# Kernel tuning notes

Measured on AMD Instinct MI355X. Metric: run time of the kernel, lower is better.

The kernel has to match this reference:

```python
import jax, jax.numpy as jnp
import numpy as np

H, DK = 12, 64  # num_heads, key_size == head_size
NEG_BIG = 1e12


def setup_inputs() -> dict:
    key = jax.random.key(0)
    ks = jax.random.split(key, 10)
    B, S, D = 4, 1024, 768
    w = lambda k, shape: jax.random.normal(k, shape, jnp.float32) * 0.02
    return {
        'q': jax.random.normal(ks[0], (B, S, D), jnp.float32),
        'k': jax.random.normal(ks[1], (B, S, D), jnp.float32),
        'v': jax.random.normal(ks[2], (B, S, D), jnp.float32),
        'Wq': w(ks[3], (D, H * DK)), 'bq': jnp.zeros((H * DK,), jnp.float32),
        'Wk': w(ks[4], (D, H * DK)), 'bk': jnp.zeros((H * DK,), jnp.float32),
        'Wv': w(ks[5], (D, H * DK)), 'bv': jnp.zeros((H * DK,), jnp.float32),
        'Wo': w(ks[6], (H * DK, H * DK)), 'bo': jnp.zeros((H * DK,), jnp.float32),
        'pos_embeddings': w(ks[7], (S, S, DK)),
        'q_mask': jnp.ones((B, S), jnp.bool_),
        'v_mask': jnp.ones((B, S), jnp.bool_),
    }


def reference(q, k, v, Wq, bq, Wk, bk, Wv, bv, Wo, bo, pos_embeddings, q_mask, v_mask):
    B, Sq, _ = q.shape
    qm = q_mask.astype(q.dtype)  # [B, Sq]
    vm = v_mask.astype(q.dtype)  # [B, Sk]

    qw = (q @ Wq + bq).reshape(B, Sq, H, DK)
    kw = (k @ Wk + bk).reshape(B, -1, H, DK)
    vw = (v @ Wv + bv).reshape(B, -1, H, DK)

    # logits + typical_relative pre-softmax bias
    a = jnp.einsum('bjhd,bkhd->bhjk', qw, kw)
    a = a + jnp.einsum('bjhd,jkd->bhjk', qw, pos_embeddings)
    a = a / jnp.asarray(DK, a.dtype) ** 0.5

    # sequence_masking on key axis (additive -1e12 on padded keys)
    a = a - (1.0 - vm[:, None, None, :]) * NEG_BIG
    a = jax.nn.softmax(a, axis=-1)

    # AV + typical_relative post-softmax bias
    o = jnp.einsum('bhjk,bkhd->bjhd', a, vw)
    o = o + jnp.einsum('bhjk,jkd->bjhd', a, pos_embeddings)

    o = o.reshape(B, Sq, H * DK) @ Wo + bo
    # sequence_masking on query axis (multiplicative)
    return o * qm[:, :, None]
```

## Files before the change

kernel.cpp:

```cpp
#include <hip/hip_runtime.h>


typedef __attribute__((ext_vector_type(8))) short bf16x8;
typedef __attribute__((ext_vector_type(4))) float f32x4;

constexpr int kS = 1024, kH = 12, kHD = 768, kBH = 48;
#define SCALE 0.125f
#define MFMA16 __builtin_amdgcn_mfma_f32_16x16x32_bf16

#define GLOAD16(gp, lp)                                                     \
  __builtin_amdgcn_global_load_lds(                                         \
      (const __attribute__((address_space(1))) void*)(gp),                  \
      (__attribute__((address_space(3))) void*)(lp), 16, 0, 0)

__device__ inline ushort f2b(float f) {
  uint u = __builtin_bit_cast(uint, f);
  u += 0x7FFFu + ((u >> 16) & 1u);
  return (ushort)(u >> 16);
}
__device__ inline float b2f(ushort h) {
  return __builtin_bit_cast(float, ((uint)h) << 16);
}

__global__ __launch_bounds__(256) void cvt_all_k(
    const float* __restrict__ s0, const float* __restrict__ s1,
    const float* __restrict__ s2, ushort* __restrict__ d0,
    ushort* __restrict__ d1, ushort* __restrict__ d2,
    const float* __restrict__ W0, const float* __restrict__ W1,
    const float* __restrict__ W2, const float* __restrict__ W3,
    ushort* __restrict__ T0, ushort* __restrict__ T1,
    ushort* __restrict__ T2, ushort* __restrict__ T3)
{
  __shared__ ushort t[64][65];
  const int tid = threadIdx.x;
  const int z = blockIdx.y;
  if (z < 3) {
    const float* in = z == 0 ? s0 : z == 1 ? s1 : s2;
    ushort* out = z == 0 ? d0 : z == 1 ? d1 : d2;
    int i = blockIdx.x * 256 + tid;
    if (i >= 393216) return;
    const float4* p = (const float4*)(in + (size_t)i * 8);
    float4 a = p[0], b = p[1];
    ushort4 o0 = { f2b(a.x), f2b(a.y), f2b(a.z), f2b(a.w) };
    ushort4 o1 = { f2b(b.x), f2b(b.y), f2b(b.z), f2b(b.w) };
    ushort* q = out + (size_t)i * 8;
    *(ushort4*)q = o0; *(ushort4*)(q + 4) = o1;
    return;
  }
  int idx = blockIdx.x;
  if (idx >= 576) return;
  int wsel = idx / 144, tno = idx % 144;
  const float* W = wsel == 0 ? W0 : wsel == 1 ? W1 : wsel == 2 ? W2 : W3;
  ushort* Wt = wsel == 0 ? T0 : wsel == 1 ? T1 : wsel == 2 ? T2 : T3;
  int r0 = (tno / 12) * 64, c0 = (tno % 12) * 64;
#pragma unroll
  for (int it = 0; it < 4; ++it) {
    int i2 = it * 256 + tid;
    int r = i2 >> 4, c4 = (i2 & 15) << 2;
    float4 v = *(const float4*)(W + (size_t)(r0 + r) * kHD + c0 + c4);
    t[c4 + 0][r] = f2b(v.x); t[c4 + 1][r] = f2b(v.y);
    t[c4 + 2][r] = f2b(v.z); t[c4 + 3][r] = f2b(v.w);
  }
  __syncthreads();
#pragma unroll
  for (int it = 0; it < 4; ++it) {
    int i2 = it * 256 + tid;
    int rr = i2 >> 4, c4 = (i2 & 15) << 2;
    ushort4 o = { t[rr][c4 + 0], t[rr][c4 + 1], t[rr][c4 + 2], t[rr][c4 + 3] };
    *(ushort4*)(Wt + (size_t)(c0 + rr) * kHD + r0 + c4) = o;
  }
}

template <int SM>
__device__ __forceinline__ void gemm_nt_body(
    const ushort* __restrict__ A, const ushort* __restrict__ Bt,
    const float* __restrict__ bias, void* __restrict__ out, int N, int K)
{
  __shared__ ushort As[64 * 40];
  __shared__ ushort Bs[64 * 40];
  int tid = threadIdx.x, w = tid >> 6, l = tid & 63, lg = l >> 4, lr = l & 15;
  int wr = w >> 1, wc = w & 1;
  int m0 = blockIdx.y * 64;
  int n0 = blockIdx.x * 64;
  int sr = tid >> 2, sc = (tid & 3) * 8;
  f32x4 acc[2][2] = {};
  for (int kb = 0; kb < K; kb += 32) {
    __syncthreads();
    *(int4*)&As[sr * 40 + sc] = *(const int4*)&A[(size_t)(m0 + sr) * K + kb + sc];
    *(int4*)&Bs[sr * 40 + sc] = *(const int4*)&Bt[(size_t)(n0 + sr) * K + kb + sc];
    __syncthreads();
    bf16x8 A0 = *(const bf16x8*)&As[(wr * 32 + lr) * 40 + 8 * lg];
    bf16x8 A1 = *(const bf16x8*)&As[(wr * 32 + 16 + lr) * 40 + 8 * lg];
    bf16x8 B0 = *(const bf16x8*)&Bs[(wc * 32 + lr) * 40 + 8 * lg];
    bf16x8 B1 = *(const bf16x8*)&Bs[(wc * 32 + 16 + lr) * 40 + 8 * lg];
    acc[0][0] = MFMA16(A0, B0, acc[0][0], 0, 0, 0);
    acc[0][1] = MFMA16(A0, B1, acc[0][1], 0, 0, 0);
    acc[1][0] = MFMA16(A1, B0, acc[1][0], 0, 0, 0);
    acc[1][1] = MFMA16(A1, B1, acc[1][1], 0, 0, 0);
  }
#pragma unroll
  for (int mf = 0; mf < 2; ++mf)
#pragma unroll
    for (int nf = 0; nf < 2; ++nf) {
      int col = n0 + wc * 32 + nf * 16 + lr;
      float bs = bias[col];
      int row0 = m0 + wr * 32 + mf * 16 + 4 * lg;
      if constexpr (SM == 0) {
        ushort* o = (ushort*)out;
#pragma unroll
        for (int r = 0; r < 4; ++r)
          o[(size_t)(row0 + r) * N + col] = f2b(acc[mf][nf][r] + bs);
      } else if constexpr (SM == 1) {
        ushort* o = (ushort*)out;
        int b = row0 >> 10, ks = row0 & 1023;
        int h = col >> 6, dd = col & 63;
        int ph = (ks & ~63) + ((((ks >> 3) & 7) ^ (dd & 7)) << 3) + (ks & 7);
        ushort4 pk = { f2b(acc[mf][nf][0] + bs), f2b(acc[mf][nf][1] + bs),
                       f2b(acc[mf][nf][2] + bs), f2b(acc[mf][nf][3] + bs) };
        *(ushort4*)(o + ((size_t)((b * kH + h) * 64 + dd)) * kS + ph) = pk;
      } else if constexpr (SM == 3) {
        ushort* o = (ushort*)out;
        int d = col & 63, hh = col >> 6;
#pragma unroll
        for (int r = 0; r < 4; ++r) {
          int row = row0 + r;
          int dp = ((((d >> 3) ^ (row & 7)) << 3)) | (d & 7);
          o[(size_t)row * N + hh * 64 + dp] = f2b(acc[mf][nf][r] + bs);
        }
      } else {
        float* o = (float*)out;
#pragma unroll
        for (int r = 0; r < 4; ++r)
          o[(size_t)(row0 + r) * N + col] = acc[mf][nf][r] + bs;
      }
    }
}

__global__ __launch_bounds__(256) void gemm_qkv_proj_k(
    const ushort* __restrict__ qb, const ushort* __restrict__ kb,
    const ushort* __restrict__ vb,
    const ushort* __restrict__ Wqt, const ushort* __restrict__ Wkt,
    const ushort* __restrict__ Wvt,
    const float* __restrict__ bq, const float* __restrict__ bk,
    const float* __restrict__ bv,
    ushort* __restrict__ qw, ushort* __restrict__ kw, ushort* __restrict__ vwT)
{
  if (blockIdx.z == 0)      gemm_nt_body<0>(qb, Wqt, bq, qw, kHD, kHD);
  else if (blockIdx.z == 1) gemm_nt_body<3>(kb, Wkt, bk, kw, kHD, kHD);
  else                      gemm_nt_body<1>(vb, Wvt, bv, vwT, kHD, kHD);
}
__global__ __launch_bounds__(256) void gemm_out_k(
    const ushort* __restrict__ ob, const ushort* __restrict__ Wot,
    const float* __restrict__ bo, float* __restrict__ out)
{
  gemm_nt_body<2>(ob, Wot, bo, out, kHD, kHD);
}

__global__ __launch_bounds__(512) void logits_pos_k(
    const ushort* __restrict__ qw, const float* __restrict__ pos,
    ushort* __restrict__ lbuf, ushort* __restrict__ posb)
{
  __shared__ ushort Qs[48 * 72];
  __shared__ ushort Ps[256 * 72];
  const int tid = threadIdx.x;
  const int w = tid >> 6, l = tid & 63, lg = l >> 4, lr = l & 15;
  const int j = blockIdx.x;
  const int jk = j & 7;

  for (int i = tid; i < 48 * 16; i += 512) {
    int bh = i >> 4, c4 = (i & 15) * 4;
    int b = bh / kH, h = bh - b * kH;
    ushort4 v = *(const ushort4*)&qw[((size_t)(b * kS + j)) * kHD + h * 64 + c4];
    *(ushort4*)&Qs[bh * 72 + c4] = v;
  }

  for (int kt = 0; kt < 4; ++kt) {
    const int k0 = kt * 256;
    __syncthreads();
    const float* psrc = pos + ((size_t)j * kS + k0) * 64;
    for (int i = tid; i < 256 * 16; i += 512) {
      int kk = i >> 4, c4 = (i & 15) * 4;
      float4 v = *(const float4*)(psrc + kk * 64 + c4);
      ushort4 o = { f2b(v.x), f2b(v.y), f2b(v.z), f2b(v.w) };
      *(ushort4*)&Ps[kk * 72 + c4] = o;
    }
    __syncthreads();

    f32x4 acc[3][2] = {};
#pragma unroll
    for (int s = 0; s < 2; ++s) {
      bf16x8 A[3], Bv[2];
#pragma unroll
      for (int mf = 0; mf < 3; ++mf)
        A[mf] = *(const bf16x8*)&Qs[(mf * 16 + lr) * 72 + s * 32 + 8 * lg];
#pragma unroll
      for (int nf = 0; nf < 2; ++nf)
        Bv[nf] = *(const bf16x8*)&Ps[(w * 32 + nf * 16 + lr) * 72 + s * 32 + 8 * lg];
#pragma unroll
      for (int mf = 0; mf < 3; ++mf)
#pragma unroll
        for (int nf = 0; nf < 2; ++nf)
          acc[mf][nf] = MFMA16(A[mf], Bv[nf], acc[mf][nf], 0, 0, 0);
    }
    for (int i = tid; i < 2048; i += 512) {
      int row = i >> 3, seg = i & 7;
      *(int4*)&posb[((size_t)j * kS + k0 + row) * 64 + seg * 8] =
          *(const int4*)&Ps[row * 72 + seg * 8];
    }
    __syncthreads();
    ushort* Ct = Ps;
#pragma unroll
    for (int mf = 0; mf < 3; ++mf)
#pragma unroll
      for (int nf = 0; nf < 2; ++nf)
#pragma unroll
        for (int r = 0; r < 4; ++r)
          Ct[(mf * 16 + 4 * lg + r) * 264 + w * 32 + nf * 16 + lr] =
              f2b(acc[mf][nf][r] * SCALE);
    __syncthreads();
    for (int i = tid; i < 48 * 32; i += 512) {
      int row = i >> 5, seg = i & 31;
      int ph = (seg >> 3) * 64 + (((seg & 7) ^ jk) << 3);
      *(int4*)&lbuf[((size_t)row * kS + j) * kS + k0 + ph] =
          *(const int4*)&Ct[row * 264 + seg * 8];
    }
  }
}

__global__ __launch_bounds__(256) void flash_qk_av_k(
    const ushort* __restrict__ qw, const ushort* __restrict__ kw,
    const ushort* __restrict__ lbuf, const ushort* __restrict__ vwT,
    ushort* __restrict__ P, float* __restrict__ o, float* __restrict__ sinv)
{
  __shared__ ushort SMEM[2 * 3 * 4096];
  const int tid = threadIdx.x;
  const int w = tid >> 6, l = tid & 63, lg = l >> 4, lr = l & 15;
  const int bid = blockIdx.x;
  const int wgid = (bid & 7) * 96 + (bid >> 3);
  const int bh = wgid >> 4, jt = wgid & 15;
  const int b = bh / kH, h = bh - b * kH;
  const int j0 = jt * 64, jw = w * 16;

  const ushort* ap = qw + ((size_t)(b * kS + j0 + jw + lr)) * kHD + h * 64 + 8 * lg;
  bf16x8 a0 = *(const bf16x8*)ap;
  bf16x8 a1 = *(const bf16x8*)(ap + 32);

  f32x4 accO[4] = {};
  float srow[4] = {0.f, 0.f, 0.f, 0.f};

  const int s0 = (w * 2) * 64 + l;
  const int s1 = s0 + 64;

#define SLOT_ISSUE(kq, buf)                                                          \
  {                                                                                  \
    ushort* Kb = SMEM + (buf) * 12288;                                               \
    ushort* Vb = Kb + 4096;                                                          \
    ushort* Lb = Vb + 4096;                                                          \
    GLOAD16(&kw[((size_t)(b * kS + (kq) + (s0 >> 3))) * kHD + h * 64 + (s0 & 7) * 8],\
            &Kb[(w * 2) * 512]);                                                     \
    GLOAD16(&kw[((size_t)(b * kS + (kq) + (s1 >> 3))) * kHD + h * 64 + (s1 & 7) * 8],\
            &Kb[(w * 2 + 1) * 512]);                                                 \
    GLOAD16(&vwT[((size_t)(bh * 64 + (s0 >> 3))) * kS + (kq) + (s0 & 7) * 8],        \
            &Vb[(w * 2) * 512]);                                                     \
    GLOAD16(&vwT[((size_t)(bh * 64 + (s1 >> 3))) * kS + (kq) + (s1 & 7) * 8],        \
            &Vb[(w * 2 + 1) * 512]);                                                 \
    GLOAD16(&lbuf[((size_t)bh * kS + j0 + (s0 >> 3)) * kS + (kq) + (s0 & 7) * 8],    \
            &Lb[(w * 2) * 512]);                                                     \
    GLOAD16(&lbuf[((size_t)bh * kS + j0 + (s1 >> 3)) * kS + (kq) + (s1 & 7) * 8],    \
            &Lb[(w * 2 + 1) * 512]);                                                 \
  }

  SLOT_ISSUE(0, 0);
  asm volatile("s_waitcnt vmcnt(0)" ::: "memory");
  __builtin_amdgcn_sched_barrier(0);
  __builtin_amdgcn_s_barrier();

  for (int kt = 0; kt < 16; ++kt) {
    const int cur = kt & 1;
    const int k0 = kt * 64;
    ushort* Kt = SMEM + cur * 12288;
    ushort* Vt = Kt + 4096;
    ushort* Lt = Vt + 4096;
    if (kt < 15) SLOT_ISSUE((kt + 1) * 64, cur ^ 1);
    if (kt > 0) {
      if (kt < 15) { asm volatile("s_waitcnt vmcnt(6)" ::: "memory"); }
      else         { asm volatile("s_waitcnt vmcnt(0)" ::: "memory"); }
      __builtin_amdgcn_sched_barrier(0);
      __builtin_amdgcn_s_barrier();
    }

    f32x4 acc[4] = {};
#pragma unroll
    for (int nf = 0; nf < 4; ++nf) {
      int kk = nf * 16 + lr, key = kk & 7;
      bf16x8 b0 = *(const bf16x8*)&Kt[kk * 64 + ((lg ^ key) << 3)];
      bf16x8 b1 = *(const bf16x8*)&Kt[kk * 64 + (((4 + lg) ^ key) << 3)];
      acc[nf] = MFMA16(a0, b0, acc[nf], 0, 0, 0);
      acc[nf] = MFMA16(a1, b1, acc[nf], 0, 0, 0);
    }
#pragma unroll
    for (int nf = 0; nf < 4; ++nf)
#pragma unroll
      for (int r = 0; r < 4; ++r) {
        int row = jw + 4 * lg + r;
        int col = nf * 16 + lr;
        int off = row * 64 + ((((col >> 3) ^ (row & 7)) << 3)) + (col & 7);
        float x = acc[nf][r] * SCALE + b2f(Lt[off]);
        float p = __expf(x);
        srow[r] += p;
        Lt[off] = f2b(p);
      }
    asm volatile("s_waitcnt lgkmcnt(0)" ::: "memory");
    __builtin_amdgcn_sched_barrier(0);
    __builtin_amdgcn_s_barrier();

    for (int i = tid; i < 512; i += 256) {
      int jr = i >> 3, pc = i & 7;
      *(int4*)&P[((size_t)bh * kS + j0 + jr) * kS + k0 + pc * 8] =
          *(const int4*)&Lt[i * 8];
    }
#pragma unroll
    for (int s = 0; s < 2; ++s) {
      int rowA = jw + lr;
      bf16x8 pa = *(const bf16x8*)&Lt[rowA * 64 + (((s * 4 + lg) ^ (rowA & 7)) << 3)];
#pragma unroll
      for (int nf = 0; nf < 4; ++nf) {
        int dd = nf * 16 + lr;
        bf16x8 bv = *(const bf16x8*)&Vt[dd * 64 + (((s * 4 + lg) ^ (dd & 7)) << 3)];
        accO[nf] = MFMA16(pa, bv, accO[nf], 0, 0, 0);
      }
    }
    asm volatile("s_waitcnt lgkmcnt(0)" ::: "memory");
    __builtin_amdgcn_sched_barrier(0);
    __builtin_amdgcn_s_barrier();
  }

#pragma unroll
  for (int off = 1; off < 16; off <<= 1)
#pragma unroll
    for (int r = 0; r < 4; ++r) srow[r] += __shfl_xor(srow[r], off);
  float inv[4];
#pragma unroll
  for (int r = 0; r < 4; ++r) inv[r] = 1.0f / srow[r];
  if (lr == 0) {
#pragma unroll
    for (int r = 0; r < 4; ++r)
      sinv[(size_t)bh * kS + j0 + jw + 4 * lg + r] = inv[r];
  }
#pragma unroll
  for (int nf = 0; nf < 4; ++nf)
#pragma unroll
    for (int r = 0; r < 4; ++r)
      o[(size_t)(b * kS + j0 + jw + 4 * lg + r) * kHD + h * 64 + nf * 16 + lr] =
          accO[nf][r] * inv[r];
}

__global__ __launch_bounds__(256) void av_pos_k(
    const ushort* __restrict__ P, const ushort* __restrict__ posb,
    const float* __restrict__ o, const float* __restrict__ sinv,
    ushort* __restrict__ ob)
{
  __shared__ ushort Bs[64 * 128];
  __shared__ ushort Pa[48][136];
  int tid = threadIdx.x, w = tid >> 6, l = tid & 63, lg = l >> 4, lr = l & 15;
  int j = blockIdx.x;
  const int jk = j & 7;
  f32x4 acc[3] = {};
  for (int kt = 0; kt < 8; ++kt) {
    int k0 = kt * 128;
    __syncthreads();
    {
      for (int i = tid; i < 1024; i += 256) {
        int kk = i >> 3, d0 = (i & 7) * 8;
        bf16x8 v = *(const bf16x8*)&posb[((size_t)j * kS + k0 + kk) * 64 + d0];
#pragma unroll
        for (int c = 0; c < 8; ++c) {
          int d = d0 + c;
          Bs[d * 128 + (kk ^ ((d & 7) << 3))] = (ushort)v[c];
        }
      }
      for (int i = tid; i < 48 * 16; i += 256) {
        int row = i >> 4, seg = i & 15;
        int4 v4 = *(const int4*)(P + ((size_t)row * kS + j) * kS + k0 + seg * 8);
        *(int4*)(&Pa[row][seg * 8]) = v4;
      }
    }
    __syncthreads();
#pragma unroll
    for (int ks = 0; ks < 4; ++ks) {
      int d = w * 16 + lr;
      bf16x8 bv = *(const bf16x8*)(&Bs[d * 128 + ((ks * 32 + 8 * lg) ^ ((d & 7) << 3))]);
      bf16x8 av[3];
      int lc = ks * 4 + lg;
      int po = (lc >> 3) * 64 + (((lc & 7) ^ jk) << 3);
#pragma unroll
      for (int mf = 0; mf < 3; ++mf)
        av[mf] = *(const bf16x8*)(&Pa[mf * 16 + lr][po]);
#pragma unroll
      for (int mf = 0; mf < 3; ++mf)
        acc[mf] = MFMA16(av[mf], bv, acc[mf], 0, 0, 0);
    }
  }
#pragma unroll
  for (int mf = 0; mf < 3; ++mf)
#pragma unroll
    for (int r = 0; r < 4; ++r) {
      int bh = mf * 16 + 4 * lg + r;
      int b = bh / kH, h = bh - b * kH;
      int d = w * 16 + lr;
      float siv = sinv[(size_t)bh * kS + j];
      size_t idx = ((size_t)(b * kS + j)) * kHD + h * 64 + d;
      ob[idx] = f2b(o[idx] + acc[mf][r] * siv);
    }
}

extern "C" void kernel_launch(void* const* d_in, const int* in_sizes, int n_in,
                              void* d_out, int out_size, void* d_ws, size_t ws_size,
                              hipStream_t stream)
{
  const float* q   = (const float*)d_in[0];
  const float* k   = (const float*)d_in[1];
  const float* v   = (const float*)d_in[2];
  const float* Wq  = (const float*)d_in[3];
  const float* bq  = (const float*)d_in[4];
  const float* Wk  = (const float*)d_in[5];
  const float* bk  = (const float*)d_in[6];
  const float* Wv  = (const float*)d_in[7];
  const float* bv  = (const float*)d_in[8];
  const float* Wo  = (const float*)d_in[9];
  const float* bo  = (const float*)d_in[10];
  const float* pos = (const float*)d_in[11];
  float* out = (float*)d_out;

  const size_t NT = (size_t)4 * kS * kHD;
  const size_t WT = (size_t)kHD * kHD;
  ushort* qb   = (ushort*)d_ws;
  ushort* kb   = qb + NT;
  ushort* vb   = kb + NT;
  ushort* qw   = vb + NT;
  ushort* kw   = qw + NT;
  ushort* vwT  = kw + NT;
  ushort* ob   = vwT + NT;
  ushort* Wqt  = ob + NT;
  ushort* Wkt  = Wqt + WT;
  ushort* Wvt  = Wkt + WT;
  ushort* Wot  = Wvt + WT;
  ushort* lb   = Wot + WT;
  ushort* Pb   = lb + (size_t)kBH * kS * kS;
  float*  o    = (float*)(Pb + (size_t)kBH * kS * kS);
  float*  sinv = o + NT;
  ushort* posb = (ushort*)(sinv + (size_t)kBH * kS);

  cvt_all_k<<<dim3(1536, 4), 256, 0, stream>>>(q, k, v, qb, kb, vb,
                                               Wq, Wk, Wv, Wo, Wqt, Wkt, Wvt, Wot);

  gemm_qkv_proj_k<<<dim3(12, 64, 3), 256, 0, stream>>>(qb, kb, vb, Wqt, Wkt, Wvt,
                                                       bq, bk, bv, qw, kw, vwT);

  logits_pos_k<<<1024, 512, 0, stream>>>(qw, pos, lb, posb);
  flash_qk_av_k<<<768, 256, 0, stream>>>(qw, kw, lb, vwT, Pb, o, sinv);
  av_pos_k<<<1024, 256, 0, stream>>>(Pb, posb, o, sinv, ob);

  gemm_out_k<<<dim3(12, 64), 256, 0, stream>>>(ob, Wot, bo, out);
}
```

Baseline: 296.5 us.

## Double-buffer P tiles via async LDS DMA and prefetch pos embeddings in av_pos_k

The flash kernel now writes P with a per-bh XOR swizzle on 8-element chunks, so av_pos_k can read it with a conflict-free pattern keyed on the row. av_pos_k loads P tiles with global_load_lds into a double buffer and prefetches the next pos-embedding tile into registers while the current tile is computed. This hides global load latency behind the MFMA work and drops one of the two syncthreads per tile. In exchange it uses more LDS and registers, and the swizzle couples the layouts of the two kernels.

```diff
diff --git a/kernel.cpp b/kernel.cpp
--- a/kernel.cpp
+++ b/kernel.cpp
@@ -240,6 +240,7 @@
   const int bh = wgid >> 4, jt = wgid & 15;
   const int b = bh / kH, h = bh - b * kH;
   const int j0 = jt * 64, jw = w * 16;
+  const int bhk = bh & 7;
 
   const ushort* ap = qw + ((size_t)(b * kS + j0 + jw + lr)) * kHD + h * 64 + 8 * lg;
   bf16x8 a0 = *(const bf16x8*)ap;
@@ -316,7 +317,7 @@
 
     for (int i = tid; i < 512; i += 256) {
       int jr = i >> 3, pc = i & 7;
-      *(int4*)&P[((size_t)bh * kS + j0 + jr) * kS + k0 + pc * 8] =
+      *(int4*)&P[((size_t)bh * kS + j0 + jr) * kS + k0 + ((pc ^ bhk) * 8)] =
           *(const int4*)&Lt[i * 8];
     }
 #pragma unroll
@@ -361,41 +362,71 @@
     ushort* __restrict__ ob)
 {
   __shared__ ushort Bs[64 * 128];
-  __shared__ ushort Pa[48][136];
+  __shared__ ushort Pa[2][48 * 128];
   int tid = threadIdx.x, w = tid >> 6, l = tid & 63, lg = l >> 4, lr = l & 15;
   int j = blockIdx.x;
-  const int jk = j & 7;
   f32x4 acc[3] = {};
+
+  const int d0 = (tid & 7) * 8;
+  const int kkb = tid >> 3;
+
+#define PA_DMA(K0, BUF)                                                        \
+  {                                                                            \
+    _Pragma("unroll")                                                          \
+    for (int c = 0; c < 3; ++c) {                                              \
+      int idx = (w * 3 + c) * 512 + l * 8;                                     \
+      int prow = idx >> 7, pcol = idx & 127;                                   \
+      GLOAD16(&P[((size_t)prow * kS + j) * kS + (K0) + pcol],                  \
+              &Pa[BUF][(w * 3 + c) * 512]);                                    \
+    }                                                                          \
+  }
+
+  bf16x8 pr0, pr1, pr2, pr3;
+  {
+    const ushort* pb = &posb[((size_t)j * kS + kkb) * 64 + d0];
+    pr0 = *(const bf16x8*)(pb);
+    pr1 = *(const bf16x8*)(pb + 32 * 64);
+    pr2 = *(const bf16x8*)(pb + 64 * 64);
+    pr3 = *(const bf16x8*)(pb + 96 * 64);
+  }
+  PA_DMA(0, 0);
+
   for (int kt = 0; kt < 8; ++kt) {
-    int k0 = kt * 128;
-    __syncthreads();
-    {
-      for (int i = tid; i < 1024; i += 256) {
-        int kk = i >> 3, d0 = (i & 7) * 8;
-        bf16x8 v = *(const bf16x8*)&posb[((size_t)j * kS + k0 + kk) * 64 + d0];
-#pragma unroll
-        for (int c = 0; c < 8; ++c) {
-          int d = d0 + c;
-          Bs[d * 128 + (kk ^ ((d & 7) << 3))] = (ushort)v[c];
-        }
-      }
-      for (int i = tid; i < 48 * 16; i += 256) {
-        int row = i >> 4, seg = i & 15;
-        int4 v4 = *(const int4*)(P + ((size_t)row * kS + j) * kS + k0 + seg * 8);
-        *(int4*)(&Pa[row][seg * 8]) = v4;
-      }
-    }
-    __syncthreads();
+    const int cur = kt & 1;
+    asm volatile("s_waitcnt vmcnt(0)" ::: "memory");
+    __builtin_amdgcn_sched_barrier(0);
+    __builtin_amdgcn_s_barrier();
+#pragma unroll
+    for (int e = 0; e < 8; ++e) {
+      int d = d0 + e;
+      int sw = (d & 7) << 3;
+      Bs[d * 128 + ((kkb +  0) ^ sw)] = (ushort)pr0[e];
+      Bs[d * 128 + ((kkb + 32) ^ sw)] = (ushort)pr1[e];
+      Bs[d * 128 + ((kkb + 64) ^ sw)] = (ushort)pr2[e];
+      Bs[d * 128 + ((kkb + 96) ^ sw)] = (ushort)pr3[e];
+    }
+    if (kt < 7) {
+      const int k0n = (kt + 1) * 128;
+      const ushort* pb = &posb[((size_t)j * kS + k0n + kkb) * 64 + d0];
+      pr0 = *(const bf16x8*)(pb);
+      pr1 = *(const bf16x8*)(pb + 32 * 64);
+      pr2 = *(const bf16x8*)(pb + 64 * 64);
+      pr3 = *(const bf16x8*)(pb + 96 * 64);
+      PA_DMA(k0n, cur ^ 1);
+    }
+    asm volatile("s_waitcnt lgkmcnt(0)" ::: "memory");
+    __builtin_amdgcn_sched_barrier(0);
+    __builtin_amdgcn_s_barrier();
 #pragma unroll
     for (int ks = 0; ks < 4; ++ks) {
       int d = w * 16 + lr;
-      bf16x8 bv = *(const bf16x8*)(&Bs[d * 128 + ((ks * 32 + 8 * lg) ^ ((d & 7) << 3))]);
+      bf16x8 bv = *(const bf16x8*)&Bs[d * 128 + ((ks * 32 + 8 * lg) ^ ((d & 7) << 3))];
       bf16x8 av[3];
       int lc = ks * 4 + lg;
-      int po = (lc >> 3) * 64 + (((lc & 7) ^ jk) << 3);
+      int po = (lc >> 3) * 64 + (((lc & 7) ^ (lr & 7)) << 3);
 #pragma unroll
       for (int mf = 0; mf < 3; ++mf)
-        av[mf] = *(const bf16x8*)(&Pa[mf * 16 + lr][po]);
+        av[mf] = *(const bf16x8*)&Pa[cur][(mf * 16 + lr) * 128 + po];
 #pragma unroll
       for (int mf = 0; mf < 3; ++mf)
         acc[mf] = MFMA16(av[mf], bv, acc[mf], 0, 0, 0);
```

New measurement: 287.1 us. -3.2%, faster.
